# Optimization experiments

Measured on AMD Instinct MI355X. Metric: run time of the kernel, lower is better.

## Reference

```python
import jax, jax.numpy as jnp
import numpy as np

B, C, H, W = 8, 512, 64, 64
CQK = C // 8  # query/key channels

def conv1x1(x, w, b):
    # x: [B,Cin,H,W], w: [Cout,Cin], b: [Cout]
    return jnp.einsum('oi,bihw->bohw', w, x) + b[None, :, None, None]

def setup_inputs() -> dict:
    key = jax.random.key(0)
    ks = jax.random.split(key, 8)
    s_in = 1.0 / np.sqrt(C)
    return {
        'x': jax.random.normal(ks[0], (B, C, H, W), dtype=jnp.float32),
        'wq': jax.random.normal(ks[1], (CQK, C), dtype=jnp.float32) * s_in,
        'bq': jax.random.normal(ks[2], (CQK,), dtype=jnp.float32) * 0.01,
        'wk': jax.random.normal(ks[3], (CQK, C), dtype=jnp.float32) * s_in,
        'bk': jax.random.normal(ks[4], (CQK,), dtype=jnp.float32) * 0.01,
        'wv': jax.random.normal(ks[5], (C, C), dtype=jnp.float32) * s_in,
        'bv': jax.random.normal(ks[6], (C,), dtype=jnp.float32) * 0.01,
        'alpha': jax.random.normal(ks[7], (1,), dtype=jnp.float32) * 0.1,
    }

def reference(x, wq, bq, wk, bk, wv, bv, alpha):
    b, c, h, w = x.shape
    n = h * w
    q = conv1x1(x, wq, bq).reshape(b, CQK, n)   # [B,C/8,N]
    k = conv1x1(x, wk, bk).reshape(b, CQK, n)   # [B,C/8,N]
    v = conv1x1(x, wv, bv).reshape(b, c, n)     # [B,C,N]
    att = jnp.einsum('bck,bcs->bks', q, k)       # [B,N,N]
    att = jax.nn.softmax(att, axis=-1)
    out = jnp.einsum('bcs,bks->bck', v, att)     # [B,C,N]
    out = out.reshape(b, c, h, w)
    return alpha[0] * out + x
```

## Files before the change

kernel.cpp:

```cpp
#include <hip/hip_runtime.h>
#include <hip/hip_bf16.h>
#include <stdint.h>

#define NB 8
#define NC 512
#define NN 4096
#define ND 64

typedef __attribute__((ext_vector_type(8))) short short8;
typedef __attribute__((ext_vector_type(4))) float f32x4;

#define LOG2E 1.44269504088896340736f

static __device__ __forceinline__ uint32_t cvt_pk_bf16(float lo, float hi) {
    uint32_t r;
    asm("v_cvt_pk_bf16_f32 %0, %1, %2" : "=v"(r) : "v"(lo), "v"(hi));
    return r;
}

static __device__ __forceinline__ void barrier_lgkm() {
    asm volatile("s_waitcnt lgkmcnt(0)" ::: "memory");
    __builtin_amdgcn_s_barrier();
    __builtin_amdgcn_sched_barrier(0);
}

__global__ __launch_bounds__(256) void wprep(
    const float* __restrict__ wq, const float* __restrict__ wk,
    const float* __restrict__ wv, unsigned short* __restrict__ Wbf)
{
    const int g = blockIdx.x * 256 + threadIdx.x;
    const int o = g >> 6;
    const int c = (g & 63) << 3;
    const float* src; float sc;
    if (o < 64)       { src = wq + (size_t)o*NC;        sc = LOG2E; }
    else if (o < 128) { src = wk + (size_t)(o-64)*NC;   sc = 1.f; }
    else              { src = wv + (size_t)(o-128)*NC;  sc = 1.f; }
    float4 a = *reinterpret_cast<const float4*>(src + c);
    float4 d = *reinterpret_cast<const float4*>(src + c + 4);
    uint4 r;
    r.x = cvt_pk_bf16(a.x*sc, a.y*sc);
    r.y = cvt_pk_bf16(a.z*sc, a.w*sc);
    r.z = cvt_pk_bf16(d.x*sc, d.y*sc);
    r.w = cvt_pk_bf16(d.z*sc, d.w*sc);
    *reinterpret_cast<uint4*>(Wbf + (size_t)o*NC + c) = r;
}

__global__ __launch_bounds__(256, 2) void qkv_proj(
    const float* __restrict__ x,
    const unsigned short* __restrict__ Wbf,
    const float* __restrict__ bq, const float* __restrict__ bk,
    const float* __restrict__ bv,
    unsigned short* __restrict__ QT, unsigned short* __restrict__ KT,
    unsigned char* __restrict__ V)
{
    const int nblk = blockIdx.x;
    const int b    = blockIdx.y;
    const int t = threadIdx.x;
    const int wid = t >> 6;
    const int l = t & 63;
    const int lg = l >> 4, lr = l & 15;
    const int n0 = nblk * 64;
    const float* xb = x + (size_t)b * NC * NN;

    __shared__ unsigned short XT[2][64][72];

    const int o_base = wid * 160;

    f32x4 acc[10][4];
    #pragma unroll
    for (int mt = 0; mt < 10; ++mt) {
        const int ob = o_base + mt*16;
        #pragma unroll
        for (int bb = 0; bb < 4; ++bb) {
            const int o = ob + lg*4 + bb;
            float bias = (ob < 64) ? bq[o]*LOG2E : (ob < 128) ? bk[o-64] : bv[o-128];
            #pragma unroll
            for (int nt = 0; nt < 4; ++nt) acc[mt][nt][bb] = bias;
        }
    }

    const int cq = (t >> 4) << 2;
    const int n4 = (t & 15) << 2;
    float4 xs0, xs1, xs2, xs3;
    auto xload = [&](int ks) {
        const float* xr = xb + (size_t)(ks*64 + cq)*NN + n0 + n4;
        xs0 = *reinterpret_cast<const float4*>(xr);
        xs1 = *reinterpret_cast<const float4*>(xr + NN);
        xs2 = *reinterpret_cast<const float4*>(xr + 2*(size_t)NN);
        xs3 = *reinterpret_cast<const float4*>(xr + 3*(size_t)NN);
    };
    auto xwrite = [&](int buf) {
        uint2 w;
        w.x = cvt_pk_bf16(xs0.x, xs1.x); w.y = cvt_pk_bf16(xs2.x, xs3.x);
        *reinterpret_cast<uint2*>(&XT[buf][n4+0][cq]) = w;
        w.x = cvt_pk_bf16(xs0.y, xs1.y); w.y = cvt_pk_bf16(xs2.y, xs3.y);
        *reinterpret_cast<uint2*>(&XT[buf][n4+1][cq]) = w;
        w.x = cvt_pk_bf16(xs0.z, xs1.z); w.y = cvt_pk_bf16(xs2.z, xs3.z);
        *reinterpret_cast<uint2*>(&XT[buf][n4+2][cq]) = w;
        w.x = cvt_pk_bf16(xs0.w, xs1.w); w.y = cvt_pk_bf16(xs2.w, xs3.w);
        *reinterpret_cast<uint2*>(&XT[buf][n4+3][cq]) = w;
    };

    xload(0);
    xwrite(0);
    __syncthreads();

    for (int ks = 0; ks < 8; ++ks) {
        const int buf = ks & 1;
        const int c0 = ks * 64;
        if (ks < 7) xload(ks + 1);
        #pragma unroll
        for (int k2 = 0; k2 < 2; ++k2) {
            short8 bf[4];
            #pragma unroll
            for (int nt = 0; nt < 4; ++nt)
                bf[nt] = *reinterpret_cast<const short8*>(&XT[buf][nt*16 + lr][k2*32 + lg*8]);
            #pragma unroll
            for (int mt = 0; mt < 10; ++mt) {
                short8 af = *reinterpret_cast<const short8*>(
                    Wbf + (size_t)(o_base + mt*16 + lr)*NC + c0 + k2*32 + lg*8);
                #pragma unroll
                for (int nt = 0; nt < 4; ++nt)
                    acc[mt][nt] = __builtin_amdgcn_mfma_f32_16x16x32_bf16(af, bf[nt], acc[mt][nt], 0, 0, 0);
            }
        }
        if (ks < 7) xwrite(buf ^ 1);
        __syncthreads();
    }

    #pragma unroll
    for (int mt = 0; mt < 10; ++mt) {
        const int ob = o_base + mt*16;
        const int ol = ob + lg*4;
        #pragma unroll
        for (int nt = 0; nt < 4; ++nt) {
            const int n = n0 + nt*16 + lr;
            if (ob < 128) {
                uint2 pk;
                pk.x = cvt_pk_bf16(acc[mt][nt][0], acc[mt][nt][1]);
                pk.y = cvt_pk_bf16(acc[mt][nt][2], acc[mt][nt][3]);
                unsigned short* dst = (ob < 64) ? (QT + ((size_t)b*NN + n)*ND + ol)
                                                : (KT + ((size_t)b*NN + n)*ND + (ol - 64));
                *reinterpret_cast<uint2*>(dst) = pk;
            } else {
                const int c = ol - 128;
                #pragma unroll
                for (int bb = 0; bb < 4; ++bb) {
                    int v8 = __builtin_amdgcn_cvt_pk_fp8_f32(acc[mt][nt][bb], 0.f, 0, false);
                    V[((size_t)b*NC + c + bb)*NN + n] = (unsigned char)(v8 & 0xff);
                }
            }
        }
    }
}

__global__ __launch_bounds__(512, 2) void attn(
    const unsigned short* __restrict__ QT,
    const unsigned short* __restrict__ KT,
    const unsigned char* __restrict__ V,
    const float* __restrict__ x,
    const float* __restrict__ alpha_p,
    float* __restrict__ out)
{
    const int bi = blockIdx.x;
    const int b  = bi & 7;
    const int n0 = (bi >> 3) * 128;
    const int t = threadIdx.x;
    const int wid = t >> 6;
    const int l = t & 63;
    const int lg = l >> 4, lr = l & 15;

    __shared__ __align__(16) unsigned short Klds[2*64*64];
    __shared__ __align__(16) unsigned char  Plds[2*128*128];
    __shared__ __align__(16) float Fb[2][128];
    __shared__ int   Flg[2][8];
    __shared__ float Ll[128];

    const unsigned short* Qb = QT + ((size_t)b*NN + n0)*ND;
    const unsigned short* Kb = KT + (size_t)b*NN*ND;
    const unsigned char*  Vb = V + ((size_t)b*NC + 64*wid)*NN;

    short8 qf0 = *reinterpret_cast<const short8*>(Qb + (size_t)(16*wid + lr)*ND + lg*8);
    short8 qf1 = *reinterpret_cast<const short8*>(Qb + (size_t)(16*wid + lr)*ND + 32 + lg*8);

    const int krow = t >> 3;
    const int kdst = krow*64 + ((8*(t & 7)) ^ (8*(krow & 7)));

    {
        short8 k0 = *reinterpret_cast<const short8*>(Kb + (size_t)t*8);
        *reinterpret_cast<short8*>(&Klds[kdst]) = k0;
    }

    f32x4 oacc[8][4];
    #pragma unroll
    for (int mt = 0; mt < 8; ++mt)
        #pragma unroll
        for (int ct = 0; ct < 4; ++ct)
            oacc[mt][ct] = f32x4{0.f, 0.f, 0.f, 0.f};

    float mrun = -1e30f, lrun = 0.f;

    long vf[4];
    #pragma unroll
    for (int ct = 0; ct < 4; ++ct)
        vf[ct] = *reinterpret_cast<const long*>(Vb + (size_t)(ct*16 + lr)*NN + 8*lg);

    barrier_lgkm();

    const int kswz = 8*(lr & 7);
    const int pswz = 8*lr;
    const int prow = (16*wid + lr) * 128;

    auto PVstep = [&](const unsigned char* pbase, int k2, int s_pref) {
        long vfn[4];
        #pragma unroll
        for (int ct = 0; ct < 4; ++ct)
            vfn[ct] = *reinterpret_cast<const long*>(
                Vb + (size_t)(ct*16 + lr)*NN + s_pref + 8*lg);
        long pf[8];
        #pragma unroll
        for (int mt = 0; mt < 8; ++mt)
            pf[mt] = *reinterpret_cast<const long*>(
                pbase + (16*mt + lr)*128 + ((k2*32 + 8*lg) ^ pswz));
        __builtin_amdgcn_s_setprio(1);
        #pragma unroll
        for (int mt = 0; mt < 8; ++mt)
            #pragma unroll
            for (int ct = 0; ct < 4; ++ct)
                oacc[mt][ct] = __builtin_amdgcn_mfma_f32_16x16x32_fp8_fp8(
                    pf[mt], vf[ct], oacc[mt][ct], 0, 0, 0);
        __builtin_amdgcn_s_setprio(0);
        #pragma unroll
        for (int ct = 0; ct < 4; ++ct) vf[ct] = vfn[ct];
    };

    {
        f32x4 sac[4];
        #pragma unroll
        for (int st8 = 0; st8 < 4; ++st8) {
            const unsigned short* kp = &Klds[(16*st8 + lr)*64];
            short8 a0 = *reinterpret_cast<const short8*>(kp + ((8*lg) ^ kswz));
            short8 a1 = *reinterpret_cast<const short8*>(kp + ((32 + 8*lg) ^ kswz));
            sac[st8] = __builtin_amdgcn_mfma_f32_16x16x32_bf16(a0, qf0, f32x4{0.f,0.f,0.f,0.f}, 0, 0, 0);
            sac[st8] = __builtin_amdgcn_mfma_f32_16x16x32_bf16(a1, qf1, sac[st8], 0, 0, 0);
        }
        short8 kr = *reinterpret_cast<const short8*>(Kb + 4096 + (size_t)t*8);

        float mx = fmaxf(fmaxf(sac[0][0], sac[0][1]), fmaxf(sac[0][2], sac[0][3]));
        #pragma unroll
        for (int st8 = 1; st8 < 4; ++st8)
            mx = fmaxf(mx, fmaxf(fmaxf(sac[st8][0], sac[st8][1]), fmaxf(sac[st8][2], sac[st8][3])));
        mx = fmaxf(mx, __shfl_xor(mx, 16));
        mx = fmaxf(mx, __shfl_xor(mx, 32));
        const float mnew = mx;
        if (l == 0) Flg[0][wid] = 1;
        if (lg == 0) Fb[0][16*wid + lr] = 0.f;
        float colsum = 0.f;
        #pragma unroll
        for (int st8 = 0; st8 < 4; ++st8) {
            float p0 = __builtin_amdgcn_exp2f(sac[st8][0] - mnew);
            float p1 = __builtin_amdgcn_exp2f(sac[st8][1] - mnew);
            float p2 = __builtin_amdgcn_exp2f(sac[st8][2] - mnew);
            float p3 = __builtin_amdgcn_exp2f(sac[st8][3] - mnew);
            colsum += (p0 + p1) + (p2 + p3);
            int d = __builtin_amdgcn_cvt_pk_fp8_f32(p0, p1, 0, false);
            d = __builtin_amdgcn_cvt_pk_fp8_f32(p2, p3, d, true);
            *reinterpret_cast<int*>(&Plds[prow + ((16*st8 + 4*lg) ^ pswz)]) = d;
        }
        colsum += __shfl_xor(colsum, 16);
        colsum += __shfl_xor(colsum, 32);
        lrun = colsum;
        mrun = mnew;
        *reinterpret_cast<short8*>(&Klds[4096 + kdst]) = kr;
    }
    barrier_lgkm();

    for (int i = 0; i < 63; ++i) {
        const int cur = i & 1, nxt = cur ^ 1;
        const unsigned char* pcur = Plds + cur*16384;
        unsigned char* pnxt = Plds + nxt*16384;
        const int s0 = i * 64;
        const int ipre = (i + 2 < 64) ? (i + 2) : 63;

        short8 kr = *reinterpret_cast<const short8*>(Kb + (size_t)ipre*4096 + t*8);

        f32x4 sn[4];
        {
            const unsigned short* kbuf = &Klds[nxt*4096];
            #pragma unroll
            for (int st8 = 0; st8 < 4; ++st8) {
                const unsigned short* kp = kbuf + (16*st8 + lr)*64;
                short8 a0 = *reinterpret_cast<const short8*>(kp + ((8*lg) ^ kswz));
                short8 a1 = *reinterpret_cast<const short8*>(kp + ((32 + 8*lg) ^ kswz));
                sn[st8] = __builtin_amdgcn_mfma_f32_16x16x32_bf16(a0, qf0, f32x4{0.f,0.f,0.f,0.f}, 0, 0, 0);
                sn[st8] = __builtin_amdgcn_mfma_f32_16x16x32_bf16(a1, qf1, sn[st8], 0, 0, 0);
            }
        }

        {
            int4 f0 = *reinterpret_cast<const int4*>(&Flg[cur][0]);
            int4 f1 = *reinterpret_cast<const int4*>(&Flg[cur][4]);
            if (f0.x | f0.y | f0.z | f0.w | f1.x | f1.y | f1.z | f1.w) {
                #pragma unroll
                for (int mt = 0; mt < 8; ++mt) {
                    float4 fr = *reinterpret_cast<const float4*>(&Fb[cur][16*mt + 4*lg]);
                    #pragma unroll
                    for (int ct = 0; ct < 4; ++ct) {
                        oacc[mt][ct][0] *= fr.x;
                        oacc[mt][ct][1] *= fr.y;
                        oacc[mt][ct][2] *= fr.z;
                        oacc[mt][ct][3] *= fr.w;
                    }
                }
            }
        }

        PVstep(pcur, 0, s0 + 32);

        float mnew, fsc, colsum = 0.f;
        {
            float mx = fmaxf(fmaxf(sn[0][0], sn[0][1]), fmaxf(sn[0][2], sn[0][3]));
            #pragma unroll
            for (int st8 = 1; st8 < 4; ++st8)
                mx = fmaxf(mx, fmaxf(fmaxf(sn[st8][0], sn[st8][1]), fmaxf(sn[st8][2], sn[st8][3])));
            mx = fmaxf(mx, __shfl_xor(mx, 16));
            mx = fmaxf(mx, __shfl_xor(mx, 32));
            bool trig = mx > mrun + 7.0f;
            unsigned long long bal = __ballot(trig);
            mnew = bal ? fmaxf(mrun, mx) : mrun;
            fsc = __builtin_amdgcn_exp2f(mrun - mnew);
            if (l == 0) Flg[nxt][wid] = (bal != 0ULL);
            if (lg == 0) Fb[nxt][16*wid + lr] = fsc;
            #pragma unroll
            for (int st8 = 0; st8 < 4; ++st8) {
                float p0 = __builtin_amdgcn_exp2f(sn[st8][0] - mnew);
                float p1 = __builtin_amdgcn_exp2f(sn[st8][1] - mnew);
                float p2 = __builtin_amdgcn_exp2f(sn[st8][2] - mnew);
                float p3 = __builtin_amdgcn_exp2f(sn[st8][3] - mnew);
                colsum += (p0 + p1) + (p2 + p3);
                int d = __builtin_amdgcn_cvt_pk_fp8_f32(p0, p1, 0, false);
                d = __builtin_amdgcn_cvt_pk_fp8_f32(p2, p3, d, true);
                *reinterpret_cast<int*>(&pnxt[prow + ((16*st8 + 4*lg) ^ pswz)]) = d;
            }
        }

        PVstep(pcur, 1, s0 + 64);

        colsum += __shfl_xor(colsum, 16);
        colsum += __shfl_xor(colsum, 32);
        lrun = lrun * fsc + colsum;
        mrun = mnew;

        *reinterpret_cast<short8*>(&Klds[cur*4096 + kdst]) = kr;

        barrier_lgkm();
    }

    {
        const unsigned char* pcur = Plds + 16384;
        const int s0 = 63 * 64;
        int4 f0 = *reinterpret_cast<const int4*>(&Flg[1][0]);
        int4 f1 = *reinterpret_cast<const int4*>(&Flg[1][4]);
        if (f0.x | f0.y | f0.z | f0.w | f1.x | f1.y | f1.z | f1.w) {
            #pragma unroll
            for (int mt = 0; mt < 8; ++mt) {
                float4 fr = *reinterpret_cast<const float4*>(&Fb[1][16*mt + 4*lg]);
                #pragma unroll
                for (int ct = 0; ct < 4; ++ct) {
                    oacc[mt][ct][0] *= fr.x;
                    oacc[mt][ct][1] *= fr.y;
                    oacc[mt][ct][2] *= fr.z;
                    oacc[mt][ct][3] *= fr.w;
                }
            }
        }
        PVstep(pcur, 0, s0 + 32);
        PVstep(pcur, 1, s0);
    }

    if (lg == 0) Ll[16*wid + lr] = lrun;
    __syncthreads();

    const float alpha = alpha_p[0];
    #pragma unroll
    for (int mt = 0; mt < 8; ++mt) {
        float4 l4 = *reinterpret_cast<const float4*>(&Ll[16*mt + 4*lg]);
        float ar0 = alpha / l4.x, ar1 = alpha / l4.y, ar2 = alpha / l4.z, ar3 = alpha / l4.w;
        #pragma unroll
        for (int ct = 0; ct < 4; ++ct) {
            const int c = 64*wid + 16*ct + lr;
            const size_t base = ((size_t)b*NC + c)*NN + n0 + 16*mt + 4*lg;
            float4 x4 = *reinterpret_cast<const float4*>(x + base);
            float4 o4;
            o4.x = oacc[mt][ct][0] * ar0 + x4.x;
            o4.y = oacc[mt][ct][1] * ar1 + x4.y;
            o4.z = oacc[mt][ct][2] * ar2 + x4.z;
            o4.w = oacc[mt][ct][3] * ar3 + x4.w;
            *reinterpret_cast<float4*>(out + base) = o4;
        }
    }
}

extern "C" void kernel_launch(void* const* d_in, const int* in_sizes, int n_in,
                              void* d_out, int out_size, void* d_ws, size_t ws_size,
                              hipStream_t stream) {
    const float* x     = (const float*)d_in[0];
    const float* wq    = (const float*)d_in[1];
    const float* bq    = (const float*)d_in[2];
    const float* wk    = (const float*)d_in[3];
    const float* bk    = (const float*)d_in[4];
    const float* wv    = (const float*)d_in[5];
    const float* bv    = (const float*)d_in[6];
    const float* alpha = (const float*)d_in[7];

    unsigned short* QT = (unsigned short*)d_ws;
    unsigned short* KT = QT + (size_t)NB*NN*ND;
    unsigned char*  V  = (unsigned char*)(KT + (size_t)NB*NN*ND);
    unsigned short* Wbf = (unsigned short*)(V + (size_t)NB*NC*NN);

    wprep<<<160, 256, 0, stream>>>(wq, wk, wv, Wbf);
    dim3 gA(64, 8);
    qkv_proj<<<gA, 256, 0, stream>>>(x, Wbf, bq, bk, bv, QT, KT, V);
    attn<<<NB * (NN/128), 512, 0, stream>>>(QT, KT, V, x, alpha, (float*)d_out);
}
```

Baseline: 221.9 us.

## Halve attention query tile to 64 with 4 waves covering 128 channels each

The attention kernel now processes 64 queries per block with 256 threads instead of 128 queries with 512 threads, doubling the grid to 512 blocks. Each wave now accumulates 128 output channels over 4 query subtiles, so PV loads twice as many V fragments per wave and half as many P fragments. K tile loading is remapped so each of the 256 threads copies two 16-byte chunks. The intent is a finer-grained grid that spreads work more evenly across CUs. The cost is that K and V are streamed once per block, so total K/V traffic from L2 and HBM doubles.

```diff
diff --git a/kernel.cpp b/kernel.cpp
--- a/kernel.cpp
+++ b/kernel.cpp
@@ -154,7 +154,7 @@
     }
 }
 
-__global__ __launch_bounds__(512, 2) void attn(
+__global__ __launch_bounds__(256, 2) void attn(
     const unsigned short* __restrict__ QT,
     const unsigned short* __restrict__ KT,
     const unsigned char* __restrict__ V,
@@ -164,45 +164,49 @@
 {
     const int bi = blockIdx.x;
     const int b  = bi & 7;
-    const int n0 = (bi >> 3) * 128;
+    const int n0 = (bi >> 3) * 64;
     const int t = threadIdx.x;
     const int wid = t >> 6;
     const int l = t & 63;
     const int lg = l >> 4, lr = l & 15;
 
     __shared__ __align__(16) unsigned short Klds[2*64*64];
-    __shared__ __align__(16) unsigned char  Plds[2*128*128];
-    __shared__ __align__(16) float Fb[2][128];
-    __shared__ int   Flg[2][8];
-    __shared__ float Ll[128];
+    __shared__ __align__(16) unsigned char  Plds[2*64*128];
+    __shared__ __align__(16) float Fb[2][64];
+    __shared__ __align__(16) int   Flg[2][4];
+    __shared__ float Ll[64];
 
     const unsigned short* Qb = QT + ((size_t)b*NN + n0)*ND;
     const unsigned short* Kb = KT + (size_t)b*NN*ND;
-    const unsigned char*  Vb = V + ((size_t)b*NC + 64*wid)*NN;
+    const unsigned char*  Vb = V + ((size_t)b*NC + 128*wid)*NN;
 
     short8 qf0 = *reinterpret_cast<const short8*>(Qb + (size_t)(16*wid + lr)*ND + lg*8);
     short8 qf1 = *reinterpret_cast<const short8*>(Qb + (size_t)(16*wid + lr)*ND + 32 + lg*8);
 
-    const int krow = t >> 3;
-    const int kdst = krow*64 + ((8*(t & 7)) ^ (8*(krow & 7)));
+    const int krow = t >> 2;
+    const int kd   = (t & 3) << 4;
+    const int kdst0 = krow*64 + ((kd)     ^ (8*(krow & 7)));
+    const int kdst1 = krow*64 + ((kd + 8) ^ (8*(krow & 7)));
 
     {
-        short8 k0 = *reinterpret_cast<const short8*>(Kb + (size_t)t*8);
-        *reinterpret_cast<short8*>(&Klds[kdst]) = k0;
-    }
-
-    f32x4 oacc[8][4];
+        short8 a = *reinterpret_cast<const short8*>(Kb + (size_t)krow*ND + kd);
+        short8 c = *reinterpret_cast<const short8*>(Kb + (size_t)krow*ND + kd + 8);
+        *reinterpret_cast<short8*>(&Klds[kdst0]) = a;
+        *reinterpret_cast<short8*>(&Klds[kdst1]) = c;
+    }
+
+    f32x4 oacc[4][8];
     #pragma unroll
-    for (int mt = 0; mt < 8; ++mt)
-        #pragma unroll
-        for (int ct = 0; ct < 4; ++ct)
+    for (int mt = 0; mt < 4; ++mt)
+        #pragma unroll
+        for (int ct = 0; ct < 8; ++ct)
             oacc[mt][ct] = f32x4{0.f, 0.f, 0.f, 0.f};
 
     float mrun = -1e30f, lrun = 0.f;
 
-    long vf[4];
+    long vf[8];
     #pragma unroll
-    for (int ct = 0; ct < 4; ++ct)
+    for (int ct = 0; ct < 8; ++ct)
         vf[ct] = *reinterpret_cast<const long*>(Vb + (size_t)(ct*16 + lr)*NN + 8*lg);
 
     barrier_lgkm();
@@ -212,26 +216,26 @@
     const int prow = (16*wid + lr) * 128;
 
     auto PVstep = [&](const unsigned char* pbase, int k2, int s_pref) {
-        long vfn[4];
-        #pragma unroll
-        for (int ct = 0; ct < 4; ++ct)
+        long vfn[8];
+        #pragma unroll
+        for (int ct = 0; ct < 8; ++ct)
             vfn[ct] = *reinterpret_cast<const long*>(
                 Vb + (size_t)(ct*16 + lr)*NN + s_pref + 8*lg);
-        long pf[8];
-        #pragma unroll
-        for (int mt = 0; mt < 8; ++mt)
+        long pf[4];
+        #pragma unroll
+        for (int mt = 0; mt < 4; ++mt)
             pf[mt] = *reinterpret_cast<const long*>(
                 pbase + (16*mt + lr)*128 + ((k2*32 + 8*lg) ^ pswz));
         __builtin_amdgcn_s_setprio(1);
         #pragma unroll
-        for (int mt = 0; mt < 8; ++mt)
-            #pragma unroll
-            for (int ct = 0; ct < 4; ++ct)
+        for (int mt = 0; mt < 4; ++mt)
+            #pragma unroll
+            for (int ct = 0; ct < 8; ++ct)
                 oacc[mt][ct] = __builtin_amdgcn_mfma_f32_16x16x32_fp8_fp8(
                     pf[mt], vf[ct], oacc[mt][ct], 0, 0, 0);
         __builtin_amdgcn_s_setprio(0);
         #pragma unroll
-        for (int ct = 0; ct < 4; ++ct) vf[ct] = vfn[ct];
+        for (int ct = 0; ct < 8; ++ct) vf[ct] = vfn[ct];
     };
 
     {
@@ -244,7 +248,8 @@
             sac[st8] = __builtin_amdgcn_mfma_f32_16x16x32_bf16(a0, qf0, f32x4{0.f,0.f,0.f,0.f}, 0, 0, 0);
             sac[st8] = __builtin_amdgcn_mfma_f32_16x16x32_bf16(a1, qf1, sac[st8], 0, 0, 0);
         }
-        short8 kr = *reinterpret_cast<const short8*>(Kb + 4096 + (size_t)t*8);
+        short8 ka = *reinterpret_cast<const short8*>(Kb + (size_t)(64 + krow)*ND + kd);
+        short8 kc = *reinterpret_cast<const short8*>(Kb + (size_t)(64 + krow)*ND + kd + 8);
 
         float mx = fmaxf(fmaxf(sac[0][0], sac[0][1]), fmaxf(sac[0][2], sac[0][3]));
         #pragma unroll
@@ -271,18 +276,20 @@
         colsum += __shfl_xor(colsum, 32);
         lrun = colsum;
         mrun = mnew;
-        *reinterpret_cast<short8*>(&Klds[4096 + kdst]) = kr;
+        *reinterpret_cast<short8*>(&Klds[4096 + kdst0]) = ka;
+        *reinterpret_cast<short8*>(&Klds[4096 + kdst1]) = kc;
     }
     barrier_lgkm();
 
     for (int i = 0; i < 63; ++i) {
         const int cur = i & 1, nxt = cur ^ 1;
-        const unsigned char* pcur = Plds + cur*16384;
-        unsigned char* pnxt = Plds + nxt*16384;
+        const unsigned char* pcur = Plds + cur*8192;
+        unsigned char* pnxt = Plds + nxt*8192;
         const int s0 = i * 64;
         const int ipre = (i + 2 < 64) ? (i + 2) : 63;
 
-        short8 kr = *reinterpret_cast<const short8*>(Kb + (size_t)ipre*4096 + t*8);
+        short8 ka = *reinterpret_cast<const short8*>(Kb + (size_t)(ipre*64 + krow)*ND + kd);
+        short8 kc = *reinterpret_cast<const short8*>(Kb + (size_t)(ipre*64 + krow)*ND + kd + 8);
 
         f32x4 sn[4];
         {
@@ -298,14 +305,13 @@
         }
 
         {
-            int4 f0 = *reinterpret_cast<const int4*>(&Flg[cur][0]);
-            int4 f1 = *reinterpret_cast<const int4*>(&Flg[cur][4]);
-            if (f0.x | f0.y | f0.z | f0.w | f1.x | f1.y | f1.z | f1.w) {
+            int4 f = *reinterpret_cast<const int4*>(&Flg[cur][0]);
+            if (f.x | f.y | f.z | f.w) {
                 #pragma unroll
-                for (int mt = 0; mt < 8; ++mt) {
+                for (int mt = 0; mt < 4; ++mt) {
                     float4 fr = *reinterpret_cast<const float4*>(&Fb[cur][16*mt + 4*lg]);
                     #pragma unroll
-                    for (int ct = 0; ct < 4; ++ct) {
+                    for (int ct = 0; ct < 8; ++ct) {
                         oacc[mt][ct][0] *= fr.x;
                         oacc[mt][ct][1] *= fr.y;
                         oacc[mt][ct][2] *= fr.z;
@@ -351,22 +357,22 @@
         lrun = lrun * fsc + colsum;
         mrun = mnew;
 
-        *reinterpret_cast<short8*>(&Klds[cur*4096 + kdst]) = kr;
+        *reinterpret_cast<short8*>(&Klds[cur*4096 + kdst0]) = ka;
+        *reinterpret_cast<short8*>(&Klds[cur*4096 + kdst1]) = kc;
 
         barrier_lgkm();
     }
 
     {
-        const unsigned char* pcur = Plds + 16384;
+        const unsigned char* pcur = Plds + 8192;
         const int s0 = 63 * 64;
-        int4 f0 = *reinterpret_cast<const int4*>(&Flg[1][0]);
-        int4 f1 = *reinterpret_cast<const int4*>(&Flg[1][4]);
-        if (f0.x | f0.y | f0.z | f0.w | f1.x | f1.y | f1.z | f1.w) {
-            #pragma unroll
-            for (int mt = 0; mt < 8; ++mt) {
+        int4 f = *reinterpret_cast<const int4*>(&Flg[1][0]);
+        if (f.x | f.y | f.z | f.w) {
+            #pragma unroll
+            for (int mt = 0; mt < 4; ++mt) {
                 float4 fr = *reinterpret_cast<const float4*>(&Fb[1][16*mt + 4*lg]);
                 #pragma unroll
-                for (int ct = 0; ct < 4; ++ct) {
+                for (int ct = 0; ct < 8; ++ct) {
                     oacc[mt][ct][0] *= fr.x;
                     oacc[mt][ct][1] *= fr.y;
                     oacc[mt][ct][2] *= fr.z;
@@ -383,12 +389,12 @@
 
     const float alpha = alpha_p[0];
     #pragma unroll
-    for (int mt = 0; mt < 8; ++mt) {
+    for (int mt = 0; mt < 4; ++mt) {
         float4 l4 = *reinterpret_cast<const float4*>(&Ll[16*mt + 4*lg]);
         float ar0 = alpha / l4.x, ar1 = alpha / l4.y, ar2 = alpha / l4.z, ar3 = alpha / l4.w;
         #pragma unroll
-        for (int ct = 0; ct < 4; ++ct) {
-            const int c = 64*wid + 16*ct + lr;
+        for (int ct = 0; ct < 8; ++ct) {
+            const int c = 128*wid + 16*ct + lr;
             const size_t base = ((size_t)b*NC + c)*NN + n0 + 16*mt + 4*lg;
             float4 x4 = *reinterpret_cast<const float4*>(x + base);
             float4 o4;
@@ -421,5 +427,5 @@
     wprep<<<160, 256, 0, stream>>>(wq, wk, wv, Wbf);
     dim3 gA(64, 8);
     qkv_proj<<<gA, 256, 0, stream>>>(x, Wbf, bq, bk, bv, QT, KT, V);
-    attn<<<NB * (NN/128), 512, 0, stream>>>(QT, KT, V, x, alpha, (float*)d_out);
-}
+    attn<<<NB * (NN/64), 256, 0, stream>>>(QT, KT, V, x, alpha, (float*)d_out);
+}
```

After: 330.3 us. 48.8% more time.

## Deepen K/P ring to four stages and sync once per two tiles

Applied to the files above, without the earlier changes.

Grows the K and P shared-memory buffers and the rescale flag/factor arrays from two slots to four. The main loop now handles two key tiles per iteration, so the workgroup barrier runs half as often and K prefetch runs further ahead. Score, softmax and rescale steps are factored into lambdas, and the prologue and epilogue now handle two tiles each. The cost is roughly double the LDS per workgroup, which may stop two 512-thread workgroups from fitting on one CU as the launch bounds request.

```diff
diff --git a/kernel.cpp b/kernel.cpp
--- a/kernel.cpp
+++ b/kernel.cpp
@@ -170,10 +170,10 @@
     const int l = t & 63;
     const int lg = l >> 4, lr = l & 15;
 
-    __shared__ __align__(16) unsigned short Klds[2*64*64];
-    __shared__ __align__(16) unsigned char  Plds[2*128*128];
-    __shared__ __align__(16) float Fb[2][128];
-    __shared__ int   Flg[2][8];
+    __shared__ __align__(16) unsigned short Klds[4*64*64];
+    __shared__ __align__(16) unsigned char  Plds[4*128*128];
+    __shared__ __align__(16) float Fb[4][128];
+    __shared__ int   Flg[4][8];
     __shared__ float Ll[128];
 
     const unsigned short* Qb = QT + ((size_t)b*NN + n0)*ND;
@@ -188,7 +188,9 @@
 
     {
         short8 k0 = *reinterpret_cast<const short8*>(Kb + (size_t)t*8);
+        short8 k1 = *reinterpret_cast<const short8*>(Kb + 4096 + (size_t)t*8);
         *reinterpret_cast<short8*>(&Klds[kdst]) = k0;
+        *reinterpret_cast<short8*>(&Klds[4096 + kdst]) = k1;
     }
 
     f32x4 oacc[8][4];
@@ -234,137 +236,58 @@
         for (int ct = 0; ct < 4; ++ct) vf[ct] = vfn[ct];
     };
 
-    {
-        f32x4 sac[4];
+    auto QKt = [&](int tile, f32x4 (&sn)[4]) {
+        const unsigned short* kbuf = &Klds[(tile & 3)*4096];
         #pragma unroll
         for (int st8 = 0; st8 < 4; ++st8) {
-            const unsigned short* kp = &Klds[(16*st8 + lr)*64];
+            const unsigned short* kp = kbuf + (16*st8 + lr)*64;
             short8 a0 = *reinterpret_cast<const short8*>(kp + ((8*lg) ^ kswz));
             short8 a1 = *reinterpret_cast<const short8*>(kp + ((32 + 8*lg) ^ kswz));
-            sac[st8] = __builtin_amdgcn_mfma_f32_16x16x32_bf16(a0, qf0, f32x4{0.f,0.f,0.f,0.f}, 0, 0, 0);
-            sac[st8] = __builtin_amdgcn_mfma_f32_16x16x32_bf16(a1, qf1, sac[st8], 0, 0, 0);
-        }
-        short8 kr = *reinterpret_cast<const short8*>(Kb + 4096 + (size_t)t*8);
-
-        float mx = fmaxf(fmaxf(sac[0][0], sac[0][1]), fmaxf(sac[0][2], sac[0][3]));
+            sn[st8] = __builtin_amdgcn_mfma_f32_16x16x32_bf16(a0, qf0, f32x4{0.f,0.f,0.f,0.f}, 0, 0, 0);
+            sn[st8] = __builtin_amdgcn_mfma_f32_16x16x32_bf16(a1, qf1, sn[st8], 0, 0, 0);
+        }
+    };
+
+    auto SMAX = [&](const f32x4 (&sn)[4], int tile) {
+        unsigned char* pb = Plds + (size_t)(tile & 3)*16384;
+        float mx = fmaxf(fmaxf(sn[0][0], sn[0][1]), fmaxf(sn[0][2], sn[0][3]));
         #pragma unroll
         for (int st8 = 1; st8 < 4; ++st8)
-            mx = fmaxf(mx, fmaxf(fmaxf(sac[st8][0], sac[st8][1]), fmaxf(sac[st8][2], sac[st8][3])));
+            mx = fmaxf(mx, fmaxf(fmaxf(sn[st8][0], sn[st8][1]), fmaxf(sn[st8][2], sn[st8][3])));
         mx = fmaxf(mx, __shfl_xor(mx, 16));
         mx = fmaxf(mx, __shfl_xor(mx, 32));
-        const float mnew = mx;
-        if (l == 0) Flg[0][wid] = 1;
-        if (lg == 0) Fb[0][16*wid + lr] = 0.f;
+        bool trig = mx > mrun + 7.0f;
+        unsigned long long bal = __ballot(trig);
+        float mnew = bal ? fmaxf(mrun, mx) : mrun;
+        float fsc = __builtin_amdgcn_exp2f(mrun - mnew);
+        if (l == 0) Flg[tile & 3][wid] = (bal != 0ULL);
+        if (lg == 0) Fb[tile & 3][16*wid + lr] = fsc;
         float colsum = 0.f;
         #pragma unroll
         for (int st8 = 0; st8 < 4; ++st8) {
-            float p0 = __builtin_amdgcn_exp2f(sac[st8][0] - mnew);
-            float p1 = __builtin_amdgcn_exp2f(sac[st8][1] - mnew);
-            float p2 = __builtin_amdgcn_exp2f(sac[st8][2] - mnew);
-            float p3 = __builtin_amdgcn_exp2f(sac[st8][3] - mnew);
+            float p0 = __builtin_amdgcn_exp2f(sn[st8][0] - mnew);
+            float p1 = __builtin_amdgcn_exp2f(sn[st8][1] - mnew);
+            float p2 = __builtin_amdgcn_exp2f(sn[st8][2] - mnew);
+            float p3 = __builtin_amdgcn_exp2f(sn[st8][3] - mnew);
             colsum += (p0 + p1) + (p2 + p3);
             int d = __builtin_amdgcn_cvt_pk_fp8_f32(p0, p1, 0, false);
             d = __builtin_amdgcn_cvt_pk_fp8_f32(p2, p3, d, true);
-            *reinterpret_cast<int*>(&Plds[prow + ((16*st8 + 4*lg) ^ pswz)]) = d;
-        }
-        colsum += __shfl_xor(colsum, 16);
-        colsum += __shfl_xor(colsum, 32);
-        lrun = colsum;
-        mrun = mnew;
-        *reinterpret_cast<short8*>(&Klds[4096 + kdst]) = kr;
-    }
-    barrier_lgkm();
-
-    for (int i = 0; i < 63; ++i) {
-        const int cur = i & 1, nxt = cur ^ 1;
-        const unsigned char* pcur = Plds + cur*16384;
-        unsigned char* pnxt = Plds + nxt*16384;
-        const int s0 = i * 64;
-        const int ipre = (i + 2 < 64) ? (i + 2) : 63;
-
-        short8 kr = *reinterpret_cast<const short8*>(Kb + (size_t)ipre*4096 + t*8);
-
-        f32x4 sn[4];
-        {
-            const unsigned short* kbuf = &Klds[nxt*4096];
-            #pragma unroll
-            for (int st8 = 0; st8 < 4; ++st8) {
-                const unsigned short* kp = kbuf + (16*st8 + lr)*64;
-                short8 a0 = *reinterpret_cast<const short8*>(kp + ((8*lg) ^ kswz));
-                short8 a1 = *reinterpret_cast<const short8*>(kp + ((32 + 8*lg) ^ kswz));
-                sn[st8] = __builtin_amdgcn_mfma_f32_16x16x32_bf16(a0, qf0, f32x4{0.f,0.f,0.f,0.f}, 0, 0, 0);
-                sn[st8] = __builtin_amdgcn_mfma_f32_16x16x32_bf16(a1, qf1, sn[st8], 0, 0, 0);
-            }
-        }
-
-        {
-            int4 f0 = *reinterpret_cast<const int4*>(&Flg[cur][0]);
-            int4 f1 = *reinterpret_cast<const int4*>(&Flg[cur][4]);
-            if (f0.x | f0.y | f0.z | f0.w | f1.x | f1.y | f1.z | f1.w) {
-                #pragma unroll
-                for (int mt = 0; mt < 8; ++mt) {
-                    float4 fr = *reinterpret_cast<const float4*>(&Fb[cur][16*mt + 4*lg]);
-                    #pragma unroll
-                    for (int ct = 0; ct < 4; ++ct) {
-                        oacc[mt][ct][0] *= fr.x;
-                        oacc[mt][ct][1] *= fr.y;
-                        oacc[mt][ct][2] *= fr.z;
-                        oacc[mt][ct][3] *= fr.w;
-                    }
-                }
-            }
-        }
-
-        PVstep(pcur, 0, s0 + 32);
-
-        float mnew, fsc, colsum = 0.f;
-        {
-            float mx = fmaxf(fmaxf(sn[0][0], sn[0][1]), fmaxf(sn[0][2], sn[0][3]));
-            #pragma unroll
-            for (int st8 = 1; st8 < 4; ++st8)
-                mx = fmaxf(mx, fmaxf(fmaxf(sn[st8][0], sn[st8][1]), fmaxf(sn[st8][2], sn[st8][3])));
-            mx = fmaxf(mx, __shfl_xor(mx, 16));
-            mx = fmaxf(mx, __shfl_xor(mx, 32));
-            bool trig = mx > mrun + 7.0f;
-            unsigned long long bal = __ballot(trig);
-            mnew = bal ? fmaxf(mrun, mx) : mrun;
-            fsc = __builtin_amdgcn_exp2f(mrun - mnew);
-            if (l == 0) Flg[nxt][wid] = (bal != 0ULL);
-            if (lg == 0) Fb[nxt][16*wid + lr] = fsc;
-            #pragma unroll
-            for (int st8 = 0; st8 < 4; ++st8) {
-                float p0 = __builtin_amdgcn_exp2f(sn[st8][0] - mnew);
-                float p1 = __builtin_amdgcn_exp2f(sn[st8][1] - mnew);
-                float p2 = __builtin_amdgcn_exp2f(sn[st8][2] - mnew);
-                float p3 = __builtin_amdgcn_exp2f(sn[st8][3] - mnew);
-                colsum += (p0 + p1) + (p2 + p3);
-                int d = __builtin_amdgcn_cvt_pk_fp8_f32(p0, p1, 0, false);
-                d = __builtin_amdgcn_cvt_pk_fp8_f32(p2, p3, d, true);
-                *reinterpret_cast<int*>(&pnxt[prow + ((16*st8 + 4*lg) ^ pswz)]) = d;
-            }
-        }
-
-        PVstep(pcur, 1, s0 + 64);
-
+            *reinterpret_cast<int*>(&pb[prow + ((16*st8 + 4*lg) ^ pswz)]) = d;
+        }
         colsum += __shfl_xor(colsum, 16);
         colsum += __shfl_xor(colsum, 32);
         lrun = lrun * fsc + colsum;
         mrun = mnew;
-
-        *reinterpret_cast<short8*>(&Klds[cur*4096 + kdst]) = kr;
-
-        barrier_lgkm();
-    }
-
-    {
-        const unsigned char* pcur = Plds + 16384;
-        const int s0 = 63 * 64;
-        int4 f0 = *reinterpret_cast<const int4*>(&Flg[1][0]);
-        int4 f1 = *reinterpret_cast<const int4*>(&Flg[1][4]);
+    };
+
+    auto RESC = [&](int tile) {
+        const int sl = tile & 3;
+        int4 f0 = *reinterpret_cast<const int4*>(&Flg[sl][0]);
+        int4 f1 = *reinterpret_cast<const int4*>(&Flg[sl][4]);
         if (f0.x | f0.y | f0.z | f0.w | f1.x | f1.y | f1.z | f1.w) {
             #pragma unroll
             for (int mt = 0; mt < 8; ++mt) {
-                float4 fr = *reinterpret_cast<const float4*>(&Fb[1][16*mt + 4*lg]);
+                float4 fr = *reinterpret_cast<const float4*>(&Fb[sl][16*mt + 4*lg]);
                 #pragma unroll
                 for (int ct = 0; ct < 4; ++ct) {
                     oacc[mt][ct][0] *= fr.x;
@@ -374,8 +297,61 @@
                 }
             }
         }
-        PVstep(pcur, 0, s0 + 32);
-        PVstep(pcur, 1, s0);
+    };
+
+    {
+        short8 k2 = *reinterpret_cast<const short8*>(Kb + 2*(size_t)4096 + t*8);
+        short8 k3 = *reinterpret_cast<const short8*>(Kb + 3*(size_t)4096 + t*8);
+        f32x4 sn[4];
+        QKt(0, sn);
+        SMAX(sn, 0);
+        QKt(1, sn);
+        SMAX(sn, 1);
+        *reinterpret_cast<short8*>(&Klds[2*4096 + kdst]) = k2;
+        *reinterpret_cast<short8*>(&Klds[3*4096 + kdst]) = k3;
+    }
+    barrier_lgkm();
+
+    for (int i = 0; i < 62; i += 2) {
+        const int s0a = i * 64;
+        const int s0b = s0a + 64;
+        const int i4 = (i + 4 < 64) ? i + 4 : 63;
+        const int i5 = (i + 5 < 64) ? i + 5 : 63;
+        const unsigned char* pA = Plds + (size_t)(i & 3)*16384;
+        const unsigned char* pB = Plds + (size_t)((i + 1) & 3)*16384;
+
+        short8 kra = *reinterpret_cast<const short8*>(Kb + (size_t)i4*4096 + t*8);
+
+        f32x4 sn[4];
+        QKt(i + 2, sn);
+        RESC(i);
+        PVstep(pA, 0, s0a + 32);
+        SMAX(sn, i + 2);
+        PVstep(pA, 1, s0a + 64);
+        *reinterpret_cast<short8*>(&Klds[(i & 3)*4096 + kdst]) = kra;
+
+        short8 krb = *reinterpret_cast<const short8*>(Kb + (size_t)i5*4096 + t*8);
+
+        QKt(i + 3, sn);
+        RESC(i + 1);
+        PVstep(pB, 0, s0b + 32);
+        SMAX(sn, i + 3);
+        PVstep(pB, 1, s0b + 64);
+        *reinterpret_cast<short8*>(&Klds[((i + 1) & 3)*4096 + kdst]) = krb;
+
+        barrier_lgkm();
+    }
+
+    {
+        const unsigned char* pA = Plds + (size_t)(62 & 3)*16384;
+        const unsigned char* pB = Plds + (size_t)(63 & 3)*16384;
+        const int s0a = 62 * 64;
+        RESC(62);
+        PVstep(pA, 0, s0a + 32);
+        PVstep(pA, 1, s0a + 64);
+        RESC(63);
+        PVstep(pB, 0, s0a + 96);
+        PVstep(pB, 1, s0a);
     }
 
     if (lg == 0) Ll[16*wid + lr] = lrun;
```

Measured after the change: 350.8 us. 1.58x slower.

## Precompute softmax row max and sum in separate stats pass before attention

Applied to the files above, without the earlier changes.

Adds a stats kernel that recomputes QK^T over all keys to get the exact per-query row max and the reciprocal of the normalizer, premultiplied by alpha. The attention kernel then uses the fixed max, which removes the online-softmax rescaling, the flag and rescale-factor LDS traffic, the ballot logic and the final row-sum reduction. The cost is a second full QK^T pass plus exp work in an extra kernel launch. The aim is a shorter main loop body for the PV-bound attention kernel.

```diff
diff --git a/kernel.cpp b/kernel.cpp
--- a/kernel.cpp
+++ b/kernel.cpp
@@ -154,12 +154,88 @@
     }
 }
 
+__global__ __launch_bounds__(512) void stats(
+    const unsigned short* __restrict__ QT,
+    const unsigned short* __restrict__ KT,
+    const float* __restrict__ alpha_p,
+    float* __restrict__ Mst, float* __restrict__ RL)
+{
+    const int bi = blockIdx.x;
+    const int b  = bi & 7;
+    const int n0 = (bi >> 3) * 128;
+    const int t = threadIdx.x;
+    const int wid = t >> 6;
+    const int l = t & 63;
+    const int lg = l >> 4, lr = l & 15;
+
+    const unsigned short* Qb = QT + ((size_t)b*NN + n0)*ND;
+    const unsigned short* Kb = KT + (size_t)b*NN*ND;
+
+    short8 qf0 = *reinterpret_cast<const short8*>(Qb + (size_t)(16*wid + lr)*ND + lg*8);
+    short8 qf1 = *reinterpret_cast<const short8*>(Qb + (size_t)(16*wid + lr)*ND + 32 + lg*8);
+
+    short8 kf[2][4][2];
+    auto ldK = [&](int tile, int buf) {
+        const unsigned short* kp = Kb + (size_t)tile*64*ND;
+        #pragma unroll
+        for (int st8 = 0; st8 < 4; ++st8) {
+            kf[buf][st8][0] = *reinterpret_cast<const short8*>(kp + (size_t)(16*st8 + lr)*ND + lg*8);
+            kf[buf][st8][1] = *reinterpret_cast<const short8*>(kp + (size_t)(16*st8 + lr)*ND + 32 + lg*8);
+        }
+    };
+
+    float mrun = -1e30f, lrun = 0.f;
+    ldK(0, 0);
+
+    #pragma unroll 2
+    for (int st = 0; st < 64; ++st) {
+        const int cb = st & 1;
+        if (st < 63) ldK(st + 1, cb ^ 1);
+
+        f32x4 sn[4];
+        #pragma unroll
+        for (int st8 = 0; st8 < 4; ++st8) {
+            sn[st8] = __builtin_amdgcn_mfma_f32_16x16x32_bf16(kf[cb][st8][0], qf0, f32x4{0.f,0.f,0.f,0.f}, 0, 0, 0);
+            sn[st8] = __builtin_amdgcn_mfma_f32_16x16x32_bf16(kf[cb][st8][1], qf1, sn[st8], 0, 0, 0);
+        }
+
+        float mx = fmaxf(fmaxf(sn[0][0], sn[0][1]), fmaxf(sn[0][2], sn[0][3]));
+        #pragma unroll
+        for (int st8 = 1; st8 < 4; ++st8)
+            mx = fmaxf(mx, fmaxf(fmaxf(sn[st8][0], sn[st8][1]), fmaxf(sn[st8][2], sn[st8][3])));
+        mx = fmaxf(mx, __shfl_xor(mx, 16));
+        mx = fmaxf(mx, __shfl_xor(mx, 32));
+
+        float mnew = fmaxf(mrun, mx);
+        float fsc = __builtin_amdgcn_exp2f(mrun - mnew);
+        float colsum = 0.f;
+        #pragma unroll
+        for (int st8 = 0; st8 < 4; ++st8) {
+            float p0 = __builtin_amdgcn_exp2f(sn[st8][0] - mnew);
+            float p1 = __builtin_amdgcn_exp2f(sn[st8][1] - mnew);
+            float p2 = __builtin_amdgcn_exp2f(sn[st8][2] - mnew);
+            float p3 = __builtin_amdgcn_exp2f(sn[st8][3] - mnew);
+            colsum += (p0 + p1) + (p2 + p3);
+        }
+        colsum += __shfl_xor(colsum, 16);
+        colsum += __shfl_xor(colsum, 32);
+        lrun = lrun * fsc + colsum;
+        mrun = mnew;
+    }
+
+    if (lg == 0) {
+        const int n = n0 + 16*wid + lr;
+        Mst[(size_t)b*NN + n] = mrun;
+        RL[(size_t)b*NN + n]  = alpha_p[0] / lrun;
+    }
+}
+
 __global__ __launch_bounds__(512, 2) void attn(
     const unsigned short* __restrict__ QT,
     const unsigned short* __restrict__ KT,
     const unsigned char* __restrict__ V,
+    const float* __restrict__ Mst, const float* __restrict__ RL,
     const float* __restrict__ x,
-    const float* __restrict__ alpha_p,
     float* __restrict__ out)
 {
     const int bi = blockIdx.x;
@@ -172,9 +248,6 @@
 
     __shared__ __align__(16) unsigned short Klds[2*64*64];
     __shared__ __align__(16) unsigned char  Plds[2*128*128];
-    __shared__ __align__(16) float Fb[2][128];
-    __shared__ int   Flg[2][8];
-    __shared__ float Ll[128];
 
     const unsigned short* Qb = QT + ((size_t)b*NN + n0)*ND;
     const unsigned short* Kb = KT + (size_t)b*NN*ND;
@@ -183,6 +256,8 @@
     short8 qf0 = *reinterpret_cast<const short8*>(Qb + (size_t)(16*wid + lr)*ND + lg*8);
     short8 qf1 = *reinterpret_cast<const short8*>(Qb + (size_t)(16*wid + lr)*ND + 32 + lg*8);
 
+    const float Mreg = Mst[(size_t)b*NN + n0 + 16*wid + lr];
+
     const int krow = t >> 3;
     const int kdst = krow*64 + ((8*(t & 7)) ^ (8*(krow & 7)));
 
@@ -197,8 +272,6 @@
         #pragma unroll
         for (int ct = 0; ct < 4; ++ct)
             oacc[mt][ct] = f32x4{0.f, 0.f, 0.f, 0.f};
-
-    float mrun = -1e30f, lrun = 0.f;
 
     long vf[4];
     #pragma unroll
@@ -234,43 +307,35 @@
         for (int ct = 0; ct < 4; ++ct) vf[ct] = vfn[ct];
     };
 
+    auto EXPK = [&](const f32x4 (&sn)[4], unsigned char* pb) {
+        #pragma unroll
+        for (int st8 = 0; st8 < 4; ++st8) {
+            float p0 = __builtin_amdgcn_exp2f(sn[st8][0] - Mreg);
+            float p1 = __builtin_amdgcn_exp2f(sn[st8][1] - Mreg);
+            float p2 = __builtin_amdgcn_exp2f(sn[st8][2] - Mreg);
+            float p3 = __builtin_amdgcn_exp2f(sn[st8][3] - Mreg);
+            int d = __builtin_amdgcn_cvt_pk_fp8_f32(p0, p1, 0, false);
+            d = __builtin_amdgcn_cvt_pk_fp8_f32(p2, p3, d, true);
+            *reinterpret_cast<int*>(&pb[prow + ((16*st8 + 4*lg) ^ pswz)]) = d;
+        }
+    };
+
+    auto QKt = [&](const unsigned short* kbuf, f32x4 (&sn)[4]) {
+        #pragma unroll
+        for (int st8 = 0; st8 < 4; ++st8) {
+            const unsigned short* kp = kbuf + (16*st8 + lr)*64;
+            short8 a0 = *reinterpret_cast<const short8*>(kp + ((8*lg) ^ kswz));
+            short8 a1 = *reinterpret_cast<const short8*>(kp + ((32 + 8*lg) ^ kswz));
+            sn[st8] = __builtin_amdgcn_mfma_f32_16x16x32_bf16(a0, qf0, f32x4{0.f,0.f,0.f,0.f}, 0, 0, 0);
+            sn[st8] = __builtin_amdgcn_mfma_f32_16x16x32_bf16(a1, qf1, sn[st8], 0, 0, 0);
+        }
+    };
+
     {
         f32x4 sac[4];
-        #pragma unroll
-        for (int st8 = 0; st8 < 4; ++st8) {
-            const unsigned short* kp = &Klds[(16*st8 + lr)*64];
-            short8 a0 = *reinterpret_cast<const short8*>(kp + ((8*lg) ^ kswz));
-            short8 a1 = *reinterpret_cast<const short8*>(kp + ((32 + 8*lg) ^ kswz));
-            sac[st8] = __builtin_amdgcn_mfma_f32_16x16x32_bf16(a0, qf0, f32x4{0.f,0.f,0.f,0.f}, 0, 0, 0);
-            sac[st8] = __builtin_amdgcn_mfma_f32_16x16x32_bf16(a1, qf1, sac[st8], 0, 0, 0);
-        }
+        QKt(&Klds[0], sac);
         short8 kr = *reinterpret_cast<const short8*>(Kb + 4096 + (size_t)t*8);
-
-        float mx = fmaxf(fmaxf(sac[0][0], sac[0][1]), fmaxf(sac[0][2], sac[0][3]));
-        #pragma unroll
-        for (int st8 = 1; st8 < 4; ++st8)
-            mx = fmaxf(mx, fmaxf(fmaxf(sac[st8][0], sac[st8][1]), fmaxf(sac[st8][2], sac[st8][3])));
-        mx = fmaxf(mx, __shfl_xor(mx, 16));
-        mx = fmaxf(mx, __shfl_xor(mx, 32));
-        const float mnew = mx;
-        if (l == 0) Flg[0][wid] = 1;
-        if (lg == 0) Fb[0][16*wid + lr] = 0.f;
-        float colsum = 0.f;
-        #pragma unroll
-        for (int st8 = 0; st8 < 4; ++st8) {
-            float p0 = __builtin_amdgcn_exp2f(sac[st8][0] - mnew);
-            float p1 = __builtin_amdgcn_exp2f(sac[st8][1] - mnew);
-            float p2 = __builtin_amdgcn_exp2f(sac[st8][2] - mnew);
-            float p3 = __builtin_amdgcn_exp2f(sac[st8][3] - mnew);
-            colsum += (p0 + p1) + (p2 + p3);
-            int d = __builtin_amdgcn_cvt_pk_fp8_f32(p0, p1, 0, false);
-            d = __builtin_amdgcn_cvt_pk_fp8_f32(p2, p3, d, true);
-            *reinterpret_cast<int*>(&Plds[prow + ((16*st8 + 4*lg) ^ pswz)]) = d;
-        }
-        colsum += __shfl_xor(colsum, 16);
-        colsum += __shfl_xor(colsum, 32);
-        lrun = colsum;
-        mrun = mnew;
+        EXPK(sac, Plds);
         *reinterpret_cast<short8*>(&Klds[4096 + kdst]) = kr;
     }
     barrier_lgkm();
@@ -285,71 +350,11 @@
         short8 kr = *reinterpret_cast<const short8*>(Kb + (size_t)ipre*4096 + t*8);
 
         f32x4 sn[4];
-        {
-            const unsigned short* kbuf = &Klds[nxt*4096];
-            #pragma unroll
-            for (int st8 = 0; st8 < 4; ++st8) {
-                const unsigned short* kp = kbuf + (16*st8 + lr)*64;
-                short8 a0 = *reinterpret_cast<const short8*>(kp + ((8*lg) ^ kswz));
-                short8 a1 = *reinterpret_cast<const short8*>(kp + ((32 + 8*lg) ^ kswz));
-                sn[st8] = __builtin_amdgcn_mfma_f32_16x16x32_bf16(a0, qf0, f32x4{0.f,0.f,0.f,0.f}, 0, 0, 0);
-                sn[st8] = __builtin_amdgcn_mfma_f32_16x16x32_bf16(a1, qf1, sn[st8], 0, 0, 0);
-            }
-        }
-
-        {
-            int4 f0 = *reinterpret_cast<const int4*>(&Flg[cur][0]);
-            int4 f1 = *reinterpret_cast<const int4*>(&Flg[cur][4]);
-            if (f0.x | f0.y | f0.z | f0.w | f1.x | f1.y | f1.z | f1.w) {
-                #pragma unroll
-                for (int mt = 0; mt < 8; ++mt) {
-                    float4 fr = *reinterpret_cast<const float4*>(&Fb[cur][16*mt + 4*lg]);
-                    #pragma unroll
-                    for (int ct = 0; ct < 4; ++ct) {
-                        oacc[mt][ct][0] *= fr.x;
-                        oacc[mt][ct][1] *= fr.y;
-                        oacc[mt][ct][2] *= fr.z;
-                        oacc[mt][ct][3] *= fr.w;
-                    }
-                }
-            }
-        }
+        QKt(&Klds[nxt*4096], sn);
 
         PVstep(pcur, 0, s0 + 32);
-
-        float mnew, fsc, colsum = 0.f;
-        {
-            float mx = fmaxf(fmaxf(sn[0][0], sn[0][1]), fmaxf(sn[0][2], sn[0][3]));
-            #pragma unroll
-            for (int st8 = 1; st8 < 4; ++st8)
-                mx = fmaxf(mx, fmaxf(fmaxf(sn[st8][0], sn[st8][1]), fmaxf(sn[st8][2], sn[st8][3])));
-            mx = fmaxf(mx, __shfl_xor(mx, 16));
-            mx = fmaxf(mx, __shfl_xor(mx, 32));
-            bool trig = mx > mrun + 7.0f;
-            unsigned long long bal = __ballot(trig);
-            mnew = bal ? fmaxf(mrun, mx) : mrun;
-            fsc = __builtin_amdgcn_exp2f(mrun - mnew);
-            if (l == 0) Flg[nxt][wid] = (bal != 0ULL);
-            if (lg == 0) Fb[nxt][16*wid + lr] = fsc;
-            #pragma unroll
-            for (int st8 = 0; st8 < 4; ++st8) {
-                float p0 = __builtin_amdgcn_exp2f(sn[st8][0] - mnew);
-                float p1 = __builtin_amdgcn_exp2f(sn[st8][1] - mnew);
-                float p2 = __builtin_amdgcn_exp2f(sn[st8][2] - mnew);
-                float p3 = __builtin_amdgcn_exp2f(sn[st8][3] - mnew);
-                colsum += (p0 + p1) + (p2 + p3);
-                int d = __builtin_amdgcn_cvt_pk_fp8_f32(p0, p1, 0, false);
-                d = __builtin_amdgcn_cvt_pk_fp8_f32(p2, p3, d, true);
-                *reinterpret_cast<int*>(&pnxt[prow + ((16*st8 + 4*lg) ^ pswz)]) = d;
-            }
-        }
-
+        EXPK(sn, pnxt);
         PVstep(pcur, 1, s0 + 64);
-
-        colsum += __shfl_xor(colsum, 16);
-        colsum += __shfl_xor(colsum, 32);
-        lrun = lrun * fsc + colsum;
-        mrun = mnew;
 
         *reinterpret_cast<short8*>(&Klds[cur*4096 + kdst]) = kr;
 
@@ -359,43 +364,24 @@
     {
         const unsigned char* pcur = Plds + 16384;
         const int s0 = 63 * 64;
-        int4 f0 = *reinterpret_cast<const int4*>(&Flg[1][0]);
-        int4 f1 = *reinterpret_cast<const int4*>(&Flg[1][4]);
-        if (f0.x | f0.y | f0.z | f0.w | f1.x | f1.y | f1.z | f1.w) {
-            #pragma unroll
-            for (int mt = 0; mt < 8; ++mt) {
-                float4 fr = *reinterpret_cast<const float4*>(&Fb[1][16*mt + 4*lg]);
-                #pragma unroll
-                for (int ct = 0; ct < 4; ++ct) {
-                    oacc[mt][ct][0] *= fr.x;
-                    oacc[mt][ct][1] *= fr.y;
-                    oacc[mt][ct][2] *= fr.z;
-                    oacc[mt][ct][3] *= fr.w;
-                }
-            }
-        }
         PVstep(pcur, 0, s0 + 32);
         PVstep(pcur, 1, s0);
     }
 
-    if (lg == 0) Ll[16*wid + lr] = lrun;
-    __syncthreads();
-
-    const float alpha = alpha_p[0];
+    const float* RLb = RL + (size_t)b*NN + n0;
     #pragma unroll
     for (int mt = 0; mt < 8; ++mt) {
-        float4 l4 = *reinterpret_cast<const float4*>(&Ll[16*mt + 4*lg]);
-        float ar0 = alpha / l4.x, ar1 = alpha / l4.y, ar2 = alpha / l4.z, ar3 = alpha / l4.w;
+        float4 r4 = *reinterpret_cast<const float4*>(RLb + 16*mt + 4*lg);
         #pragma unroll
         for (int ct = 0; ct < 4; ++ct) {
             const int c = 64*wid + 16*ct + lr;
             const size_t base = ((size_t)b*NC + c)*NN + n0 + 16*mt + 4*lg;
             float4 x4 = *reinterpret_cast<const float4*>(x + base);
             float4 o4;
-            o4.x = oacc[mt][ct][0] * ar0 + x4.x;
-            o4.y = oacc[mt][ct][1] * ar1 + x4.y;
-            o4.z = oacc[mt][ct][2] * ar2 + x4.z;
-            o4.w = oacc[mt][ct][3] * ar3 + x4.w;
+            o4.x = oacc[mt][ct][0] * r4.x + x4.x;
+            o4.y = oacc[mt][ct][1] * r4.y + x4.y;
+            o4.z = oacc[mt][ct][2] * r4.z + x4.z;
+            o4.w = oacc[mt][ct][3] * r4.w + x4.w;
             *reinterpret_cast<float4*>(out + base) = o4;
         }
     }
@@ -417,9 +403,12 @@
     unsigned short* KT = QT + (size_t)NB*NN*ND;
     unsigned char*  V  = (unsigned char*)(KT + (size_t)NB*NN*ND);
     unsigned short* Wbf = (unsigned short*)(V + (size_t)NB*NC*NN);
+    float* Mst = (float*)(Wbf + (size_t)640*NC);
+    float* RLp = Mst + (size_t)NB*NN;
 
     wprep<<<160, 256, 0, stream>>>(wq, wk, wv, Wbf);
     dim3 gA(64, 8);
     qkv_proj<<<gA, 256, 0, stream>>>(x, Wbf, bq, bk, bv, QT, KT, V);
-    attn<<<NB * (NN/128), 512, 0, stream>>>(QT, KT, V, x, alpha, (float*)d_out);
-}
+    stats<<<NB * (NN/128), 512, 0, stream>>>(QT, KT, alpha, Mst, RLp);
+    attn<<<NB * (NN/128), 512, 0, stream>>>(QT, KT, V, Mst, RLp, x, (float*)d_out);
+}
```

Result: slower. 319.7 us (+44.1%).
